# Kernel tuning notes

Measured on AMD Instinct MI355X. Metric: run time of the kernel, lower is better.

## Reference

```python
import jax, jax.numpy as jnp
import numpy as np

D_MODEL = 768
D_STATE = 16
D_CONV = 4
EXPAND = 2
D_INNER = D_MODEL * EXPAND  # 1536
B = 2
T = 8192
ALPHA = 0.9  # hard-coded EMA coefficient in _parallel_scan


def setup_inputs() -> dict:
    key = jax.random.key(0)
    ks = jax.random.split(key, 12)
    s = 0.02
    return {
        "x": jax.random.normal(ks[0], (B, T, D_MODEL), jnp.float32),
        "in_w": jax.random.normal(ks[1], (D_MODEL, 2 * D_INNER), jnp.float32) * s,
        "in_b": jnp.zeros((2 * D_INNER,), jnp.float32),
        "conv_w": jax.random.normal(ks[2], (D_INNER, 1, D_CONV), jnp.float32) * s,  # OIH, depthwise
        "conv_b": jnp.zeros((D_INNER,), jnp.float32),
        "xp_w": jax.random.normal(ks[3], (D_INNER, 2 * D_STATE), jnp.float32) * s,
        "xp_b": jnp.zeros((2 * D_STATE,), jnp.float32),
        "dt_w": jax.random.normal(ks[4], (D_STATE, D_INNER), jnp.float32) * s,
        "dt_b": jnp.zeros((D_INNER,), jnp.float32),
        "D_param": jnp.ones((D_INNER,), jnp.float32),
        "out_w": jax.random.normal(ks[5], (D_INNER, D_MODEL), jnp.float32) * s,
        "out_b": jnp.zeros((D_MODEL,), jnp.float32),
    }


def _forward(x, in_w, in_b, conv_w, conv_b, xp_w, xp_b, dt_w, dt_b, D_param, out_w, out_b):
    # in_proj: [B,T,D] -> [B,T,2*d_inner]
    xz = x @ in_w + in_b
    x_inner, z = jnp.split(xz, 2, axis=-1)

    # Causal depthwise conv1d (torch pads both sides by d_conv-1 then slices [:T],
    # which is equivalent to left-pad d_conv-1, right-pad 0)
    xc = jnp.transpose(x_inner, (0, 2, 1))  # [B, d_inner, T]
    xc = jax.lax.conv_general_dilated(
        xc, conv_w, window_strides=(1,), padding=[(D_CONV - 1, 0)],
        dimension_numbers=("NCH", "OIH", "NCH"), feature_group_count=D_INNER,
    ) + conv_b[None, :, None]
    x_conv = jax.nn.silu(jnp.transpose(xc, (0, 2, 1)))  # [B, T, d_inner]

    # NOTE: original computes x_proj/dt_proj/A_bar here, but _parallel_scan ignores
    # A_bar/B_ssm/C_ssm entirely, so they are dead code w.r.t. the output (omitted).

    # Serial EMA scan: h_t = alpha*h_{t-1} + (1-alpha)*x_conv_t
    def step(h, xt):
        h = ALPHA * h + (1.0 - ALPHA) * xt
        return h, h

    h0 = jnp.zeros((x.shape[0], D_INNER), x_conv.dtype)
    _, hs = jax.lax.scan(step, h0, jnp.transpose(x_conv, (1, 0, 2)))  # [T,B,d_inner]
    scan_out = jnp.transpose(hs, (1, 0, 2))

    y = x_conv * D_param + scan_out
    y = y * jax.nn.silu(z)
    return y @ out_w + out_b  # dropout is identity at inference


def reference(x, in_w, in_b, conv_w, conv_b, xp_w, xp_b, dt_w, dt_b, D_param, out_w, out_b):
    return _forward(x, in_w, in_b, conv_w, conv_b, xp_w, xp_b, dt_w, dt_b, D_param, out_w, out_b)
```

## Files before the change

kernel.cpp:

```cpp
#include <hip/hip_runtime.h>

#define D_MODEL 768
#define D_INNER 1536
#define NXZ     3072
#define BATCH   2
#define SEQ     8192
#define MTOT    (BATCH*SEQ)
#define WARM    64

typedef _Float16 v8h __attribute__((ext_vector_type(8)));
typedef _Float16 v4h __attribute__((ext_vector_type(4)));
typedef float    v4f __attribute__((ext_vector_type(4)));
typedef _Float16 f16;

__global__ void k_cvt(const float* __restrict__ in, f16* __restrict__ out, int n4) {
  int i = blockIdx.x * blockDim.x + threadIdx.x;
  if (i < n4) {
    float4 v = reinterpret_cast<const float4*>(in)[i];
    v4h o;
    o[0] = (f16)v.x; o[1] = (f16)v.y; o[2] = (f16)v.z; o[3] = (f16)v.w;
    reinterpret_cast<v4h*>(out)[i] = o;
  }
}

__global__ void k_transpose_cvt(const float* __restrict__ in, f16* __restrict__ out,
                                int R, int C) {
  __shared__ float tile[32][33];
  int c0 = blockIdx.x * 32, r0 = blockIdx.y * 32;
  int tx = threadIdx.x, ty = threadIdx.y;
#pragma unroll
  for (int i = 0; i < 32; i += 8)
    tile[ty + i][tx] = in[(long)(r0 + ty + i) * C + (c0 + tx)];
  __syncthreads();
#pragma unroll
  for (int i = 0; i < 32; i += 8)
    out[(long)(c0 + ty + i) * R + (r0 + tx)] = (f16)tile[tx][ty + i];
}

__device__ __forceinline__ void gload_lds16(const void* g, void* l) {
  __builtin_amdgcn_global_load_lds((const __attribute__((address_space(1))) void*)g,
                                   (__attribute__((address_space(3))) void*)l, 16, 0, 0);
}

template <bool F16OUT>
__launch_bounds__(256, 2)
__global__ void k_gemm_bt(const f16* __restrict__ A, const f16* __restrict__ Bt,
                          const float* __restrict__ bias, void* __restrict__ Cv,
                          int M, int N, int K) {
  __shared__ f16 As[128][32];
  __shared__ f16 Bs[128][32];
  const int tid  = threadIdx.x;
  const int lane = tid & 63;
  const int wave = tid >> 6;
  const int wm   = (wave >> 1) * 64;
  const int wn   = (wave & 1) * 64;
  const int m16  = lane & 15;
  const int quad = lane >> 4;
  const int rsw  = (m16 >> 1) & 3;
  const long m0 = (long)blockIdx.y * 128;
  const long n0 = (long)blockIdx.x * 128;

  v4f acc[4][4];
#pragma unroll
  for (int i = 0; i < 4; i++)
#pragma unroll
    for (int j = 0; j < 4; j++)
#pragma unroll
      for (int r = 0; r < 4; r++) acc[i][j][r] = 0.f;

  const int srow = wave * 16 + (lane >> 2);
  const int scol = (((lane & 3) ^ ((lane >> 3) & 3)) << 3);
  const f16* Ag = A  + (m0 + srow) * (long)K + scol;
  const f16* Bg = Bt + (n0 + srow) * (long)K + scol;
  f16* AsW0 = &As[wave * 16][0];
  f16* AsW1 = &As[64 + wave * 16][0];
  f16* BsW0 = &Bs[wave * 16][0];
  f16* BsW1 = &Bs[64 + wave * 16][0];

  for (int k0 = 0; k0 < K; k0 += 32) {
    gload_lds16(Ag,                 AsW0);
    gload_lds16(Ag + (long)64 * K,  AsW1);
    gload_lds16(Bg,                 BsW0);
    gload_lds16(Bg + (long)64 * K,  BsW1);
    Ag += 32; Bg += 32;
    __syncthreads();
    v8h af[4], bfr[4];
#pragma unroll
    for (int i = 0; i < 4; i++) af[i]  = *(const v8h*)&As[wm + i * 16 + m16][(quad ^ rsw) * 8];
#pragma unroll
    for (int j = 0; j < 4; j++) bfr[j] = *(const v8h*)&Bs[wn + j * 16 + m16][(quad ^ rsw) * 8];
#pragma unroll
    for (int i = 0; i < 4; i++)
#pragma unroll
      for (int j = 0; j < 4; j++)
        acc[i][j] = __builtin_amdgcn_mfma_f32_16x16x32_f16(af[i], bfr[j], acc[i][j], 0, 0, 0);
    __syncthreads();
  }

#pragma unroll
  for (int i = 0; i < 4; i++) {
#pragma unroll
    for (int j = 0; j < 4; j++) {
      const long n = n0 + wn + j * 16 + m16;
      const float bv = bias[n];
#pragma unroll
      for (int r = 0; r < 4; r++) {
        const long m = m0 + wm + i * 16 + quad * 4 + r;
        float v = acc[i][j][r] + bv;
        if (F16OUT) ((f16*)Cv)[m * N + n] = (f16)v;
        else        ((float*)Cv)[m * N + n] = v;
      }
    }
  }
}

__global__ void k_conv_scan(const f16* __restrict__ xz, const float* __restrict__ conv_w,
                            const float* __restrict__ conv_b, const float* __restrict__ Dp_,
                            f16* __restrict__ y) {
  __shared__ f16 xs[64][256];
  __shared__ f16 zs[64][256];
  const int tid = threadIdx.x;
  const int c0  = blockIdx.y * 256;
  const int c   = c0 + tid;
  const int b   = blockIdx.z;
  const int t0  = blockIdx.x * 128;
  const float w0 = conv_w[c * 4 + 0], w1 = conv_w[c * 4 + 1];
  const float w2 = conv_w[c * 4 + 2], w3 = conv_w[c * 4 + 3];
  const float cb = conv_b[c], Dp = Dp_[c];
  const long mb = (long)b * SEQ;

  float xm3 = 0.f, xm2 = 0.f, xm1 = 0.f, h = 0.f;
  const int ts = t0 - WARM;
  if (t0 > 0) {
    xm3 = (float)xz[(mb + ts - 3) * (long)NXZ + c];
    xm2 = (float)xz[(mb + ts - 2) * (long)NXZ + c];
    xm1 = (float)xz[(mb + ts - 1) * (long)NXZ + c];
  }

  for (int p = 0; p < 3; ++p) {
    const int tp = ts + p * 64;
    __syncthreads();
    if (tp >= 0) {
#pragma unroll
      for (int j = 0; j < 8; ++j) {
        const int idx = j * 256 + tid, row = idx >> 5, col = (idx & 31) << 3;
        *(v8h*)&xs[row][col] = *(const v8h*)&xz[(mb + tp + row) * (long)NXZ + c0 + col];
      }
      if (p > 0) {
#pragma unroll
        for (int j = 0; j < 8; ++j) {
          const int idx = j * 256 + tid, row = idx >> 5, col = (idx & 31) << 3;
          *(v8h*)&zs[row][col] = *(const v8h*)&xz[(mb + tp + row) * (long)NXZ + D_INNER + c0 + col];
        }
      }
    }
    __syncthreads();
    if (tp < 0) continue;
    if (p == 0) {
      for (int tl = 0; tl < 64; ++tl) {
        float xt = (float)xs[tl][tid];
        float u = w0 * xm3 + w1 * xm2 + w2 * xm1 + w3 * xt + cb;
        h = 0.9f * h + 0.1f * (u / (1.f + __expf(-u)));
        xm3 = xm2; xm2 = xm1; xm1 = xt;
      }
    } else {
      f16* yo = y + (mb + tp) * (long)D_INNER + c;
      for (int tl = 0; tl < 64; ++tl) {
        float xt = (float)xs[tl][tid];
        float u = w0 * xm3 + w1 * xm2 + w2 * xm1 + w3 * xt + cb;
        float v = u / (1.f + __expf(-u));
        h = 0.9f * h + 0.1f * v;
        float zv = (float)zs[tl][tid];
        float g = zv / (1.f + __expf(-zv));
        yo[(long)tl * D_INNER] = (f16)((v * Dp + h) * g);
        xm3 = xm2; xm2 = xm1; xm1 = xt;
      }
    }
  }
}

extern "C" void kernel_launch(void* const* d_in, const int* in_sizes, int n_in,
                              void* d_out, int out_size, void* d_ws, size_t ws_size,
                              hipStream_t stream) {
  const float* x       = (const float*)d_in[0];
  const float* in_w    = (const float*)d_in[1];
  const float* in_b    = (const float*)d_in[2];
  const float* conv_w  = (const float*)d_in[3];
  const float* conv_b  = (const float*)d_in[4];
  const float* D_param = (const float*)d_in[9];
  const float* out_w   = (const float*)d_in[10];
  const float* out_b   = (const float*)d_in[11];
  float* out = (float*)d_out;

  char* p = (char*)d_ws;
  f16* xb    = (f16*)p; p += (size_t)MTOT * D_MODEL * 2;
  f16* wInT  = (f16*)p; p += (size_t)NXZ * D_MODEL * 2;
  f16* wOutT = (f16*)p; p += (size_t)D_MODEL * D_INNER * 2;
  f16* xzb   = (f16*)p; p += (size_t)MTOT * NXZ * 2;
  f16* yb    = (f16*)p; p += (size_t)MTOT * D_INNER * 2;

  k_cvt<<<(MTOT * D_MODEL / 4 + 255) / 256, 256, 0, stream>>>(x, xb, MTOT * D_MODEL / 4);
  k_transpose_cvt<<<dim3(NXZ / 32, D_MODEL / 32), dim3(32, 8), 0, stream>>>(in_w, wInT, D_MODEL, NXZ);
  k_transpose_cvt<<<dim3(D_MODEL / 32, D_INNER / 32), dim3(32, 8), 0, stream>>>(out_w, wOutT, D_INNER, D_MODEL);

  k_gemm_bt<true><<<dim3(NXZ / 128, MTOT / 128), 256, 0, stream>>>(xb, wInT, in_b, xzb, MTOT, NXZ, D_MODEL);

  k_conv_scan<<<dim3(SEQ / 128, D_INNER / 256, BATCH), 256, 0, stream>>>(xzb, conv_w, conv_b, D_param, yb);

  k_gemm_bt<false><<<dim3(D_MODEL / 128, MTOT / 128), 256, 0, stream>>>(yb, wOutT, out_b, out, MTOT, D_MODEL, D_INNER);
}
```

Measured before the change: 348.3 us.

## Load GEMM B operand directly to registers and halve conv-scan LDS tiles

The GEMM kernel no longer stages the B (weight) tile in shared memory. Each wave loads its B fragments straight from global memory into registers, double-buffered one k-step ahead. Occupancy is raised to 3 blocks per CU. Separately, the conv-scan kernel processes time in 32-row chunks instead of 64, which halves its LDS footprint. The aim is to cut LDS traffic and usage and improve occupancy, but B reuse across waves is lost, so global and L2 traffic for weights doubles and register pressure rises.

```diff
diff --git a/kernel.cpp b/kernel.cpp
--- a/kernel.cpp
+++ b/kernel.cpp
@@ -7,6 +7,7 @@
 #define SEQ     8192
 #define MTOT    (BATCH*SEQ)
 #define WARM    64
+#define TP      32
 
 typedef _Float16 v8h __attribute__((ext_vector_type(8)));
 typedef _Float16 v4h __attribute__((ext_vector_type(4)));
@@ -43,12 +44,11 @@
 }
 
 template <bool F16OUT>
-__launch_bounds__(256, 2)
+__launch_bounds__(256, 3)
 __global__ void k_gemm_bt(const f16* __restrict__ A, const f16* __restrict__ Bt,
                           const float* __restrict__ bias, void* __restrict__ Cv,
                           int M, int N, int K) {
   __shared__ f16 As[128][32];
-  __shared__ f16 Bs[128][32];
   const int tid  = threadIdx.x;
   const int lane = tid & 63;
   const int wave = tid >> 6;
@@ -70,30 +70,36 @@
 
   const int srow = wave * 16 + (lane >> 2);
   const int scol = (((lane & 3) ^ ((lane >> 3) & 3)) << 3);
-  const f16* Ag = A  + (m0 + srow) * (long)K + scol;
-  const f16* Bg = Bt + (n0 + srow) * (long)K + scol;
+  const f16* Ag = A + (m0 + srow) * (long)K + scol;
   f16* AsW0 = &As[wave * 16][0];
   f16* AsW1 = &As[64 + wave * 16][0];
-  f16* BsW0 = &Bs[wave * 16][0];
-  f16* BsW1 = &Bs[64 + wave * 16][0];
+
+  const f16* Bf = Bt + (n0 + wn + m16) * (long)K + quad * 8;
+  v8h bcur[4], bnxt[4];
+#pragma unroll
+  for (int j = 0; j < 4; j++) bcur[j] = *(const v8h*)(Bf + (long)(j * 16) * K);
+#pragma unroll
+  for (int j = 0; j < 4; j++) bnxt[j] = *(const v8h*)(Bf + (long)(j * 16) * K + 32);
 
   for (int k0 = 0; k0 < K; k0 += 32) {
-    gload_lds16(Ag,                 AsW0);
-    gload_lds16(Ag + (long)64 * K,  AsW1);
-    gload_lds16(Bg,                 BsW0);
-    gload_lds16(Bg + (long)64 * K,  BsW1);
-    Ag += 32; Bg += 32;
-    __syncthreads();
-    v8h af[4], bfr[4];
-#pragma unroll
-    for (int i = 0; i < 4; i++) af[i]  = *(const v8h*)&As[wm + i * 16 + m16][(quad ^ rsw) * 8];
-#pragma unroll
-    for (int j = 0; j < 4; j++) bfr[j] = *(const v8h*)&Bs[wn + j * 16 + m16][(quad ^ rsw) * 8];
+    gload_lds16(Ag,                AsW0);
+    gload_lds16(Ag + (long)64 * K, AsW1);
+    Ag += 32;
+    __syncthreads();
+    v8h af[4];
+#pragma unroll
+    for (int i = 0; i < 4; i++) af[i] = *(const v8h*)&As[wm + i * 16 + m16][(quad ^ rsw) * 8];
 #pragma unroll
     for (int i = 0; i < 4; i++)
 #pragma unroll
       for (int j = 0; j < 4; j++)
-        acc[i][j] = __builtin_amdgcn_mfma_f32_16x16x32_f16(af[i], bfr[j], acc[i][j], 0, 0, 0);
+        acc[i][j] = __builtin_amdgcn_mfma_f32_16x16x32_f16(af[i], bcur[j], acc[i][j], 0, 0, 0);
+#pragma unroll
+    for (int j = 0; j < 4; j++) bcur[j] = bnxt[j];
+    if (k0 + 64 < K) {
+#pragma unroll
+      for (int j = 0; j < 4; j++) bnxt[j] = *(const v8h*)(Bf + (long)(j * 16) * K + k0 + 64);
+    }
     __syncthreads();
   }
 
@@ -117,8 +123,8 @@
 __global__ void k_conv_scan(const f16* __restrict__ xz, const float* __restrict__ conv_w,
                             const float* __restrict__ conv_b, const float* __restrict__ Dp_,
                             f16* __restrict__ y) {
-  __shared__ f16 xs[64][256];
-  __shared__ f16 zs[64][256];
+  __shared__ f16 xs[TP][256];
+  __shared__ f16 zs[TP][256];
   const int tid = threadIdx.x;
   const int c0  = blockIdx.y * 256;
   const int c   = c0 + tid;
@@ -137,18 +143,18 @@
     xm1 = (float)xz[(mb + ts - 1) * (long)NXZ + c];
   }
 
-  for (int p = 0; p < 3; ++p) {
-    const int tp = ts + p * 64;
+  for (int p = 0; p < 6; ++p) {
+    const int tp = ts + p * TP;
     __syncthreads();
     if (tp >= 0) {
 #pragma unroll
-      for (int j = 0; j < 8; ++j) {
+      for (int j = 0; j < 4; ++j) {
         const int idx = j * 256 + tid, row = idx >> 5, col = (idx & 31) << 3;
         *(v8h*)&xs[row][col] = *(const v8h*)&xz[(mb + tp + row) * (long)NXZ + c0 + col];
       }
-      if (p > 0) {
-#pragma unroll
-        for (int j = 0; j < 8; ++j) {
+      if (p >= 2) {
+#pragma unroll
+        for (int j = 0; j < 4; ++j) {
           const int idx = j * 256 + tid, row = idx >> 5, col = (idx & 31) << 3;
           *(v8h*)&zs[row][col] = *(const v8h*)&xz[(mb + tp + row) * (long)NXZ + D_INNER + c0 + col];
         }
@@ -156,8 +162,8 @@
     }
     __syncthreads();
     if (tp < 0) continue;
-    if (p == 0) {
-      for (int tl = 0; tl < 64; ++tl) {
+    if (p < 2) {
+      for (int tl = 0; tl < TP; ++tl) {
         float xt = (float)xs[tl][tid];
         float u = w0 * xm3 + w1 * xm2 + w2 * xm1 + w3 * xt + cb;
         h = 0.9f * h + 0.1f * (u / (1.f + __expf(-u)));
@@ -165,7 +171,7 @@
       }
     } else {
       f16* yo = y + (mb + tp) * (long)D_INNER + c;
-      for (int tl = 0; tl < 64; ++tl) {
+      for (int tl = 0; tl < TP; ++tl) {
         float xt = (float)xs[tl][tid];
         float u = w0 * xm3 + w1 * xm2 + w2 * xm1 + w3 * xt + cb;
         float v = u / (1.f + __expf(-u));
```

After: 444.5 us. 27.6% more time.
